# Kernel tuning notes

Hardware: AMD Instinct MI355X
Metric: run time of the kernel (lower is better)

The kernel has to match this reference:

```python
import jax, jax.numpy as jnp
import numpy as np

NUM_HEADS = 16
BN_EPS = 1e-3  # tf.layers.BatchNormalization default epsilon


def _z_norm(a, axis, scale):
    mu = jnp.mean(a, axis=axis, keepdims=True)
    sd = jnp.std(a, axis=axis, keepdims=True)
    return (a - mu) / (sd * scale + 1e-10)


def setup_inputs() -> dict:
    key = jax.random.key(0)
    ks = jax.random.split(key, 12)
    B, S, D = 4, 1024, 1024
    w = lambda k: jax.random.normal(k, (D, D), dtype=jnp.float32) * 0.02
    return {
        'q': jax.random.normal(ks[0], (B, S, D), dtype=jnp.float32),
        'k': jax.random.normal(ks[1], (B, S, D), dtype=jnp.float32),
        'v': jax.random.normal(ks[2], (B, S, D), dtype=jnp.float32),
        'mask': jax.random.randint(ks[3], (B, 1, S, S), 0, 2, dtype=jnp.int32),
        'is_training': 0,
        'q_gamma': jnp.ones((D,), jnp.float32),
        'q_beta': jnp.zeros((D,), jnp.float32),
        'q_mean': jax.random.normal(ks[4], (D,), dtype=jnp.float32) * 0.1,
        'q_var': jnp.ones((D,), jnp.float32),
        'Wq': w(ks[5]), 'bq': jnp.zeros((D,), jnp.float32),
        'Wqq': w(ks[6]), 'bqq': jnp.zeros((D,), jnp.float32),
        'Wo': w(ks[7]), 'bo': jnp.zeros((D,), jnp.float32),
    }


def reference(q, k, v, mask, is_training, q_gamma, q_beta, q_mean, q_var,
              Wq, bq, Wqq, bqq, Wo, bo):
    B, S, D = q.shape
    H = NUM_HEADS
    dh = D // H
    # BatchNorm (inference mode: call() passes no training flag -> moving stats)
    x = (q - q_mean) * jax.lax.rsqrt(q_var + BN_EPS) * q_gamma + q_beta
    # q = wqq(relu(wq(.)))  (k/v projections are dead: call() sets k = v = q)
    x = jax.nn.relu(x @ Wq + bq)
    x = x @ Wqq + bqq
    qh = x.reshape(B, S, H, dh).transpose(0, 2, 1, 3)  # [B,H,S,dh]
    logits = jnp.einsum('bhqd,bhkd->bhqk', qh, qh) / jnp.sqrt(jnp.float32(dh))
    logits = logits + mask.astype(logits.dtype) * -1e9
    attn = jax.nn.softmax(logits, axis=3)  # [B,H,S,S]
    last = jnp.mean(logits, axis=-1, keepdims=True)        # [B,H,S,1]
    last2 = jnp.mean(logits, axis=(2, 3), keepdims=True)   # [B,H,1,1]
    w_within = jax.nn.softmax(_z_norm(last, 2, 2), axis=2)   # softmax over queries
    w_betw = jax.nn.softmax(_z_norm(last2, 1, 2), axis=1)    # softmax over heads
    attn = attn * w_within * w_betw
    out = jnp.einsum('bhqk,bhkd->bhqd', attn, qh)           # v == qh
    out = out.transpose(0, 2, 1, 3).reshape(B, S, D)
    out = out @ Wo + bo
    return out, attn
```

## Files before the change

### kernel.cpp

```cpp
#include <hip/hip_runtime.h>
#include <math.h>


constexpr int Bz = 4, S = 1024, D = 1024, H = 16, DH = 64;
constexpr int N_ROWS = Bz * S;
#define BN_EPS 1e-3f
#define NEG_BIG -1e9f

typedef __attribute__((ext_vector_type(8))) short bf16x8;
typedef __attribute__((ext_vector_type(8))) unsigned short u16x8;
typedef __attribute__((ext_vector_type(4))) float f32x4;

__device__ inline unsigned short f2bf(float f) {
  union { float f; unsigned int u; } v; v.f = f;
  unsigned int u = v.u;
  return (unsigned short)((u + 0x7FFFu + ((u >> 16) & 1u)) >> 16);
}
__device__ inline float bf2f(unsigned short h) {
  union { unsigned int u; float f; } v; v.u = ((unsigned int)h) << 16;
  return v.f;
}
__device__ inline bf16x8 pack8(float4 a, float4 b) {
  bf16x8 v;
  v[0] = (short)f2bf(a.x); v[1] = (short)f2bf(a.y);
  v[2] = (short)f2bf(a.z); v[3] = (short)f2bf(a.w);
  v[4] = (short)f2bf(b.x); v[5] = (short)f2bf(b.y);
  v[6] = (short)f2bf(b.z); v[7] = (short)f2bf(b.w);
  return v;
}
__device__ inline float4 bnf(float4 f, float4 s, float4 sh) {
  return make_float4(fmaf(f.x, s.x, sh.x), fmaf(f.y, s.y, sh.y),
                     fmaf(f.z, s.z, sh.z), fmaf(f.w, s.w, sh.w));
}

__global__ __launch_bounds__(256)
void k_prep_all(const float* __restrict__ W0, const float* __restrict__ W1,
                const float* __restrict__ W2, unsigned short* __restrict__ T0,
                unsigned short* __restrict__ T1, unsigned short* __restrict__ T2,
                const float* __restrict__ gamma, const float* __restrict__ beta,
                const float* __restrict__ mean, const float* __restrict__ var,
                float* __restrict__ bnsc, float* __restrict__ bnsh,
                const int* __restrict__ mask, float* __restrict__ n_cnt2,
                float* __restrict__ cs) {
  __shared__ float Ls[64][65];
  const int bid = blockIdx.x, t = threadIdx.x;
  if (bid < 768) {
    const int z = bid >> 8, rem = bid & 255;
    const float* W = z == 0 ? W0 : (z == 1 ? W1 : W2);
    unsigned short* T = z == 0 ? T0 : (z == 1 ? T1 : T2);
    const int k0 = (rem & 15) * 64, n0 = (rem >> 4) * 64;
    {
      const int r = t >> 2, c0 = (t & 3) * 16;
#pragma unroll
      for (int i = 0; i < 4; ++i) {
        float4 f = *(const float4*)&W[(size_t)(k0 + r) * 1024 + n0 + c0 + 4 * i];
        Ls[r][c0 + 4 * i] = f.x; Ls[r][c0 + 4 * i + 1] = f.y;
        Ls[r][c0 + 4 * i + 2] = f.z; Ls[r][c0 + 4 * i + 3] = f.w;
      }
    }
    __syncthreads();
    {
      const int d = t >> 2, c = t & 3;
      u16x8 o0, o1;
#pragma unroll
      for (int i = 0; i < 8; ++i) {
        o0[i] = f2bf(Ls[c * 16 + i][d]);
        o1[i] = f2bf(Ls[c * 16 + 8 + i][d]);
      }
      unsigned short* dst = &T[(size_t)(n0 + d) * 1024 + k0 + c * 16];
      *(u16x8*)dst = o0;
      *(u16x8*)(dst + 8) = o1;
    }
  } else if (bid < 832) {
    const int id = bid - 768;
    const int row = id * 64 + (t >> 2);
    const int4* mp = (const int4*)&mask[(size_t)row * 1024 + (t & 3) * 256];
    int s = 0;
#pragma unroll 8
    for (int i = 0; i < 64; ++i) { int4 m = mp[i]; s += (m.x + m.y) + (m.z + m.w); }
    s += __shfl_xor(s, 1, 64);
    s += __shfl_xor(s, 2, 64);
    if ((t & 3) == 0) n_cnt2[row] = (float)s;
  } else if (bid < 836) {
    const int id = bid - 832;
    *(float4*)&cs[id * 1024 + t * 4] = make_float4(0.f, 0.f, 0.f, 0.f);
  } else {
    const int i = (bid - 836) * 256 + t;
    float sc = gamma[i] * rsqrtf(var[i] + BN_EPS);
    bnsc[i] = sc;
    bnsh[i] = beta[i] - mean[i] * sc;
  }
}

template<int AMODE, bool RELU, bool OUTBF, bool CSUM>
__global__ __launch_bounds__(256)
void k_gemm2n(const void* __restrict__ Asrc, const unsigned short* __restrict__ BT,
              const float* __restrict__ bias, void* __restrict__ C,
              const float* __restrict__ bnsc, const float* __restrict__ bnsh,
              float* __restrict__ cs) {
  __shared__ unsigned short As[128 * 64];
  __shared__ unsigned short Bs[64 * 64];
  const int t = threadIdx.x;
  const int w = t >> 6, l = t & 63, l15 = l & 15, l4 = l >> 4;
  const int m0 = blockIdx.x * 128, n0 = blockIdx.y * 64;
  const int wm = (w >> 1) * 64, wn = (w & 1) * 32;

  f32x4 acc[4][2];
#pragma unroll
  for (int i = 0; i < 4; ++i)
#pragma unroll
    for (int j = 0; j < 2; ++j) acc[i][j] = (f32x4){0.f, 0.f, 0.f, 0.f};

  for (int k0 = 0; k0 < 1024; k0 += 64) {
    __syncthreads();
#pragma unroll
    for (int i = 0; i < 4; ++i) {
      const int c = i * 256 + t, row = c >> 3, slot = c & 7;
      bf16x8 v;
      if (AMODE == 0) {
        v = *(const bf16x8*)&((const unsigned short*)Asrc)[(size_t)(m0 + row) * 1024 + k0 + slot * 8];
      } else {
        const float* ap = &((const float*)Asrc)[(size_t)(m0 + row) * 1024 + k0 + slot * 8];
        float4 f0 = *(const float4*)ap, f1 = *(const float4*)(ap + 4);
        float4 s0 = *(const float4*)&bnsc[k0 + slot * 8];
        float4 s1 = *(const float4*)&bnsc[k0 + slot * 8 + 4];
        float4 h0 = *(const float4*)&bnsh[k0 + slot * 8];
        float4 h1 = *(const float4*)&bnsh[k0 + slot * 8 + 4];
        v = pack8(bnf(f0, s0, h0), bnf(f1, s1, h1));
      }
      *(bf16x8*)((char*)As + row * 128 + ((slot * 16) ^ ((row & 7) << 4))) = v;
    }
#pragma unroll
    for (int i = 0; i < 2; ++i) {
      const int c = i * 256 + t, row = c >> 3, slot = c & 7;
      bf16x8 v = *(const bf16x8*)&BT[(size_t)(n0 + row) * 1024 + k0 + slot * 8];
      *(bf16x8*)((char*)Bs + row * 128 + ((slot * 16) ^ ((row & 7) << 4))) = v;
    }
    __syncthreads();
    bf16x8 af[4][2], bfr[2][2];
#pragma unroll
    for (int bm = 0; bm < 4; ++bm) {
      const int r = wm + bm * 16 + l15;
#pragma unroll
      for (int kk = 0; kk < 2; ++kk)
        af[bm][kk] = *(const bf16x8*)((const char*)As + r * 128 +
                                      ((kk * 64 + l4 * 16) ^ ((r & 7) << 4)));
    }
#pragma unroll
    for (int bn = 0; bn < 2; ++bn) {
      const int r = wn + bn * 16 + l15;
#pragma unroll
      for (int kk = 0; kk < 2; ++kk)
        bfr[bn][kk] = *(const bf16x8*)((const char*)Bs + r * 128 +
                                       ((kk * 64 + l4 * 16) ^ ((r & 7) << 4)));
    }
#pragma unroll
    for (int bm = 0; bm < 4; ++bm)
#pragma unroll
      for (int bn = 0; bn < 2; ++bn) {
        acc[bm][bn] = __builtin_amdgcn_mfma_f32_16x16x32_bf16(af[bm][0], bfr[bn][0], acc[bm][bn], 0, 0, 0);
        acc[bm][bn] = __builtin_amdgcn_mfma_f32_16x16x32_bf16(af[bm][1], bfr[bn][1], acc[bm][bn], 0, 0, 0);
      }
  }
  float bv[2];
#pragma unroll
  for (int bn = 0; bn < 2; ++bn) bv[bn] = bias[n0 + wn + bn * 16 + l15];
  float csum[2] = {0.f, 0.f};
#pragma unroll
  for (int bm = 0; bm < 4; ++bm)
#pragma unroll
    for (int bn = 0; bn < 2; ++bn)
#pragma unroll
      for (int r = 0; r < 4; ++r) {
        float v = acc[bm][bn][r] + bv[bn];
        if (RELU) v = fmaxf(v, 0.f);
        if (CSUM) csum[bn] += v;
        const size_t idx = (size_t)(m0 + wm + bm * 16 + l4 * 4 + r) * 1024 +
                           n0 + wn + bn * 16 + l15;
        if (OUTBF) ((unsigned short*)C)[idx] = f2bf(v);
        else ((float*)C)[idx] = v;
      }
  if (CSUM) {
#pragma unroll
    for (int bn = 0; bn < 2; ++bn) {
      float s = csum[bn];
      s += __shfl_xor(s, 16, 64);
      s += __shfl_xor(s, 32, 64);
      if (l4 == 0)
        atomicAdd(&cs[(m0 >> 10) * 1024 + n0 + wn + bn * 16 + l15], s);
    }
  }
}

__global__ __launch_bounds__(256)
void k_cvt(const unsigned short* __restrict__ xqb, unsigned short* __restrict__ qhT) {
  __shared__ unsigned short Ls[64][72];
  const int t = threadIdx.x;
  const int b = blockIdx.x >> 4;
  const int sb = (blockIdx.x & 15) * 64;
  const int h = blockIdx.y;
  {
    const int r = t >> 2, c0 = (t & 3) * 16;
    const unsigned short* src = &xqb[(size_t)(b * 1024 + sb + r) * 1024 + h * 64 + c0];
    u16x8 a = *(const u16x8*)src;
    u16x8 b8 = *(const u16x8*)(src + 8);
    *(u16x8*)&Ls[r][c0] = a;
    *(u16x8*)&Ls[r][c0 + 8] = b8;
  }
  __syncthreads();
  {
    const int d = t >> 2, c = t & 3;
    u16x8 o0, o1;
#pragma unroll
    for (int i = 0; i < 8; ++i) {
      o0[i] = Ls[c * 16 + i][d];
      o1[i] = Ls[c * 16 + 8 + i][d];
    }
    unsigned short* dst = &qhT[(size_t)((b * 16 + h) * 64 + d) * 1024 + sb + c * 16];
    *(u16x8*)dst = o0;
    *(u16x8*)(dst + 8) = o1;
  }
}

template<int PASS>
__global__ __launch_bounds__(256)
void k_attn6(const unsigned short* __restrict__ xqb, const int* __restrict__ mask,
             const unsigned short* __restrict__ qhT, const float* __restrict__ w_row,
             float* __restrict__ attn, unsigned short* __restrict__ pvb,
             float* __restrict__ denom) {
  __shared__ unsigned short Ks[2][128 * 64];
  __shared__ unsigned short Pst[PASS ? 4 * 16 * 64 : 8];

  const int t = threadIdx.x;
  const int w = t >> 6, l = t & 63;
  const int l15 = l & 15, l4 = l >> 4;
  const int q0 = blockIdx.x * 64;
  const int h = blockIdx.y, b = blockIdx.z;
  const int bh = b * 16 + h;

  bf16x8 qa0, qa1;
  {
    const unsigned short* qp =
        &xqb[(size_t)(b * 1024 + q0 + w * 16 + l15) * 1024 + h * 64 + l4 * 8];
    qa0 = *(const bf16x8*)qp;
    qa1 = *(const bf16x8*)(qp + 32);
  }

  float wsc[4];
  if (PASS == 1) {
#pragma unroll
    for (int r = 0; r < 4; ++r)
      wsc[r] = w_row[(size_t)bh * 1024 + q0 + w * 16 + l4 * 4 + r];
  }

  float dsum[4] = {0.f, 0.f, 0.f, 0.f};
  f32x4 vacc[4];
#pragma unroll
  for (int c = 0; c < 4; ++c) vacc[c] = (f32x4){0.f, 0.f, 0.f, 0.f};

  const int srow = t >> 3, sslot = t & 7;
  const int sswz = (sslot * 16) ^ ((srow & 7) << 4);
  const size_t sga = (size_t)(b * 1024 + srow) * 1024 + h * 64 + sslot * 8;

  bf16x8 s0, s1, s2, s3;
  s0 = *(const bf16x8*)&xqb[sga];
  s1 = *(const bf16x8*)&xqb[sga + 32 * 1024];
  s2 = *(const bf16x8*)&xqb[sga + 64 * 1024];
  s3 = *(const bf16x8*)&xqb[sga + 96 * 1024];
  *(bf16x8*)((char*)Ks[0] + srow * 128 + sswz) = s0;
  *(bf16x8*)((char*)Ks[0] + (srow + 32) * 128 + sswz) = s1;
  *(bf16x8*)((char*)Ks[0] + (srow + 64) * 128 + sswz) = s2;
  *(bf16x8*)((char*)Ks[0] + (srow + 96) * 128 + sswz) = s3;
  s0 = *(const bf16x8*)&xqb[sga + 128 * 1024];
  s1 = *(const bf16x8*)&xqb[sga + 160 * 1024];
  s2 = *(const bf16x8*)&xqb[sga + 192 * 1024];
  s3 = *(const bf16x8*)&xqb[sga + 224 * 1024];

  for (int ti = 0; ti < 8; ++ti) {
    __syncthreads();
    const int cur = ti & 1;
    if (ti < 7) {
      *(bf16x8*)((char*)Ks[cur ^ 1] + srow * 128 + sswz) = s0;
      *(bf16x8*)((char*)Ks[cur ^ 1] + (srow + 32) * 128 + sswz) = s1;
      *(bf16x8*)((char*)Ks[cur ^ 1] + (srow + 64) * 128 + sswz) = s2;
      *(bf16x8*)((char*)Ks[cur ^ 1] + (srow + 96) * 128 + sswz) = s3;
    }
    if (ti < 6) {
      const size_t base = sga + (size_t)(ti + 2) * 131072;
      s0 = *(const bf16x8*)&xqb[base];
      s1 = *(const bf16x8*)&xqb[base + 32 * 1024];
      s2 = *(const bf16x8*)&xqb[base + 64 * 1024];
      s3 = *(const bf16x8*)&xqb[base + 96 * 1024];
    }
    const int k0 = ti * 128;

#pragma unroll
    for (int half = 0; half < 2; ++half) {
      const int koff = k0 + half * 64;
      f32x4 lacc[4];
#pragma unroll
      for (int c = 0; c < 4; ++c) {
        const int r = half * 64 + c * 16 + l15;
        const char* kb = (const char*)Ks[cur] + r * 128;
        const int rsw = (r & 7) << 4;
        bf16x8 kb0 = *(const bf16x8*)(kb + ((l4 * 16) ^ rsw));
        bf16x8 kb1 = *(const bf16x8*)(kb + ((64 + l4 * 16) ^ rsw));
        f32x4 z = (f32x4){0.f, 0.f, 0.f, 0.f};
        z = __builtin_amdgcn_mfma_f32_16x16x32_bf16(qa0, kb0, z, 0, 0, 0);
        z = __builtin_amdgcn_mfma_f32_16x16x32_bf16(qa1, kb1, z, 0, 0, 0);
        lacc[c] = z;
      }

      int mrr[4][4];
#pragma unroll
      for (int c = 0; c < 4; ++c)
#pragma unroll
        for (int r = 0; r < 4; ++r)
          mrr[c][r] = mask[(size_t)(b * 1024 + q0 + w * 16 + l4 * 4 + r) * 1024 +
                           koff + c * 16 + l15];

#pragma unroll
      for (int c = 0; c < 4; ++c) {
#pragma unroll
        for (int r = 0; r < 4; ++r) {
          float p = __expf(fmaf((float)mrr[c][r], NEG_BIG, lacc[c][r] * 0.125f));
          if (PASS == 0) {
            dsum[r] += p;
          } else {
            attn[(size_t)(bh * 1024 + q0 + w * 16 + l4 * 4 + r) * 1024 +
                 koff + c * 16 + l15] = p * wsc[r];
            const int qq = l4 * 4 + r;
            *(unsigned short*)((char*)&Pst[w * 1024] + qq * 128 +
                               (((c * 16 + l15) * 2) ^ ((qq & 7) << 4))) = f2bf(p);
          }
        }
      }

      if (PASS == 1) {
#pragma unroll
        for (int kk = 0; kk < 2; ++kk) {
          const char* pb = (const char*)&Pst[w * 1024] + l15 * 128;
          bf16x8 pa = *(const bf16x8*)(pb + ((kk * 64 + l4 * 16) ^ ((l15 & 7) << 4)));
#pragma unroll
          for (int c = 0; c < 4; ++c) {
            bf16x8 vb = *(const bf16x8*)&qhT[(size_t)(bh * 64 + c * 16 + l15) * 1024 +
                                             koff + kk * 32 + l4 * 8];
            vacc[c] = __builtin_amdgcn_mfma_f32_16x16x32_bf16(pa, vb, vacc[c], 0, 0, 0);
          }
        }
      }
    }
  }

  if (PASS == 0) {
#pragma unroll
    for (int r = 0; r < 4; ++r) {
      float d2 = dsum[r];
#pragma unroll
      for (int m = 1; m < 16; m <<= 1) d2 += __shfl_xor(d2, m, 64);
      if (l15 == 0)
        denom[(size_t)bh * 1024 + q0 + w * 16 + l4 * 4 + r] = d2;
    }
  } else {
#pragma unroll
    for (int c = 0; c < 4; ++c)
#pragma unroll
      for (int r = 0; r < 4; ++r)
        pvb[(size_t)(b * 1024 + q0 + w * 16 + l4 * 4 + r) * 1024 +
            h * 64 + c * 16 + l15] = f2bf(vacc[c][r] * wsc[r]);
  }
}

__global__ __launch_bounds__(256)
void k_wwithin(const unsigned short* __restrict__ xqb, const float* __restrict__ cs,
               const float* __restrict__ n_cnt2, const float* __restrict__ denom,
               float* __restrict__ w_row) {
  __shared__ double buf[1024];
  __shared__ double red[256];
  __shared__ float csl[64];
  __shared__ double sh_mu, sh_sd, sh_zm, sh_es;
  const int bh = blockIdx.x, t = threadIdx.x;
  const int base = bh << 10;
  const int b = bh >> 4, h = bh & 15;
  const int nbase = b << 10;
  if (t < 64) csl[t] = cs[b * 1024 + h * 64 + t];
  __syncthreads();
  double part = 0;
  for (int j = 0; j < 4; ++j) {
    const int q2 = t + j * 256;
    const unsigned short* xr = &xqb[(size_t)(b * 1024 + q2) * 1024 + h * 64];
    float s = 0.f;
#pragma unroll
    for (int dd = 0; dd < 64; dd += 8) {
      u16x8 xv = *(const u16x8*)&xr[dd];
      s += bf2f(xv[0]) * csl[dd]     + bf2f(xv[1]) * csl[dd + 1] +
           bf2f(xv[2]) * csl[dd + 2] + bf2f(xv[3]) * csl[dd + 3] +
           bf2f(xv[4]) * csl[dd + 4] + bf2f(xv[5]) * csl[dd + 5] +
           bf2f(xv[6]) * csl[dd + 6] + bf2f(xv[7]) * csl[dd + 7];
    }
    double last = ((double)(s * 0.125f) - 1e9 * (double)n_cnt2[nbase + q2]) * (1.0 / 1024.0);
    buf[q2] = last; part += last;
  }
  red[t] = part; __syncthreads();
  for (int s2 = 128; s2 > 0; s2 >>= 1) { if (t < s2) red[t] += red[t + s2]; __syncthreads(); }
  if (t == 0) sh_mu = red[0] * (1.0 / 1024.0);
  __syncthreads();
  const double mu = sh_mu;
  part = 0;
  for (int q2 = t; q2 < 1024; q2 += 256) { double d = buf[q2] - mu; part += d * d; }
  red[t] = part; __syncthreads();
  for (int s2 = 128; s2 > 0; s2 >>= 1) { if (t < s2) red[t] += red[t + s2]; __syncthreads(); }
  if (t == 0) sh_sd = sqrt(red[0] * (1.0 / 1024.0));
  __syncthreads();
  const double dn = sh_sd * 2.0 + 1e-10;
  part = -1e300;
  for (int q2 = t; q2 < 1024; q2 += 256) {
    double z = (buf[q2] - mu) / dn;
    buf[q2] = z;
    part = fmax(part, z);
  }
  red[t] = part; __syncthreads();
  for (int s2 = 128; s2 > 0; s2 >>= 1) { if (t < s2) red[t] = fmax(red[t], red[t + s2]); __syncthreads(); }
  if (t == 0) sh_zm = red[0];
  __syncthreads();
  const double zm = sh_zm;
  part = 0;
  for (int q2 = t; q2 < 1024; q2 += 256) {
    double e = exp(buf[q2] - zm);
    buf[q2] = e; part += e;
  }
  red[t] = part; __syncthreads();
  for (int s2 = 128; s2 > 0; s2 >>= 1) { if (t < s2) red[t] += red[t + s2]; __syncthreads(); }
  if (t == 0) sh_es = red[0];
  __syncthreads();
  const double tot = sh_es;
  for (int q2 = t; q2 < 1024; q2 += 256) {
    w_row[base + q2] = (float)(buf[q2] / tot * 0.0625 / (double)denom[base + q2]);
  }
}

extern "C" void kernel_launch(void* const* d_in, const int* in_sizes, int n_in,
                              void* d_out, int out_size, void* d_ws, size_t ws_size,
                              hipStream_t stream) {
  const float* q      = (const float*)d_in[0];
  const int*   mask   = (const int*)d_in[3];
  const float* q_gamma = (const float*)d_in[5];
  const float* q_beta  = (const float*)d_in[6];
  const float* q_mean  = (const float*)d_in[7];
  const float* q_var   = (const float*)d_in[8];
  const float* Wq  = (const float*)d_in[9];
  const float* bq  = (const float*)d_in[10];
  const float* Wqq = (const float*)d_in[11];
  const float* bqq = (const float*)d_in[12];
  const float* Wo  = (const float*)d_in[13];
  const float* bo  = (const float*)d_in[14];

  float* out  = (float*)d_out;
  float* attn = (float*)d_out + (size_t)N_ROWS * D;
  unsigned short* xqb = (unsigned short*)d_out;

  char* ws = (char*)d_ws;
  unsigned short* x1b = (unsigned short*)(ws);
  unsigned short* qhT = (unsigned short*)(ws + (8u << 20));
  unsigned short* pvb = (unsigned short*)(ws + (16u << 20));
  unsigned short* WqT  = (unsigned short*)(ws + (32u << 20));
  unsigned short* WqqT = (unsigned short*)(ws + (34u << 20));
  unsigned short* WoT  = (unsigned short*)(ws + (36u << 20));
  float* cs     = (float*)(ws + (38u << 20));
  float* denom  = cs + 4096;
  float* w_row  = denom + 65536;
  float* n_cnt2 = w_row + 65536;
  float* bnsc   = n_cnt2 + 4096;
  float* bnsh   = bnsc + 1024;

  k_prep_all<<<840, 256, 0, stream>>>(Wq, Wqq, Wo, WqT, WqqT, WoT,
                                      q_gamma, q_beta, q_mean, q_var, bnsc, bnsh,
                                      mask, n_cnt2, cs);

  dim3 gg(32, 16);
  k_gemm2n<1, true, true, false><<<gg, 256, 0, stream>>>(q, WqT, bq, x1b, bnsc, bnsh, nullptr);
  k_gemm2n<0, false, true, true><<<gg, 256, 0, stream>>>(x1b, WqqT, bqq, xqb, nullptr, nullptr, cs);

  k_cvt<<<dim3(64, 16), 256, 0, stream>>>(xqb, qhT);

  dim3 ga(16, 16, 4);
  k_attn6<0><<<ga, 256, 0, stream>>>(xqb, mask, nullptr, nullptr, nullptr, nullptr, denom);
  k_wwithin<<<Bz * H, 256, 0, stream>>>(xqb, cs, n_cnt2, denom, w_row);
  k_attn6<1><<<ga, 256, 0, stream>>>(xqb, mask, qhT, w_row, attn, pvb, nullptr);

  k_gemm2n<0, false, false, false><<<gg, 256, 0, stream>>>(pvb, WoT, bo, out, nullptr, nullptr, nullptr);
}
```

Measured before the change: 248.4 us.

## Use direct global-to-LDS loads for GEMM and attention K tiles

```diff
diff --git a/kernel.cpp b/kernel.cpp
--- a/kernel.cpp
+++ b/kernel.cpp
@@ -31,6 +31,13 @@
 __device__ inline float4 bnf(float4 f, float4 s, float4 sh) {
   return make_float4(fmaf(f.x, s.x, sh.x), fmaf(f.y, s.y, sh.y),
                      fmaf(f.z, s.z, sh.z), fmaf(f.w, s.w, sh.w));
+}
+
+__device__ __forceinline__ void gl16(const void* g, void* l) {
+  __builtin_amdgcn_global_load_lds(
+      (const __attribute__((address_space(1))) unsigned int*)(unsigned long long)g,
+      (__attribute__((address_space(3))) unsigned int*)(unsigned int)(unsigned long long)l,
+      16, 0, 0);
 }
 
 __global__ __launch_bounds__(256)
@@ -116,9 +123,10 @@
 #pragma unroll
     for (int i = 0; i < 4; ++i) {
       const int c = i * 256 + t, row = c >> 3, slot = c & 7;
-      bf16x8 v;
       if (AMODE == 0) {
-        v = *(const bf16x8*)&((const unsigned short*)Asrc)[(size_t)(m0 + row) * 1024 + k0 + slot * 8];
+        const char* gs = (const char*)&((const unsigned short*)Asrc)[(size_t)(m0 + row) * 1024 + k0] +
+                         ((slot * 16) ^ ((row & 7) << 4));
+        gl16(gs, (char*)As + (i * 256 + w * 64) * 16);
       } else {
         const float* ap = &((const float*)Asrc)[(size_t)(m0 + row) * 1024 + k0 + slot * 8];
         float4 f0 = *(const float4*)ap, f1 = *(const float4*)(ap + 4);
@@ -126,15 +134,16 @@
         float4 s1 = *(const float4*)&bnsc[k0 + slot * 8 + 4];
         float4 h0 = *(const float4*)&bnsh[k0 + slot * 8];
         float4 h1 = *(const float4*)&bnsh[k0 + slot * 8 + 4];
-        v = pack8(bnf(f0, s0, h0), bnf(f1, s1, h1));
-      }
-      *(bf16x8*)((char*)As + row * 128 + ((slot * 16) ^ ((row & 7) << 4))) = v;
+        bf16x8 v = pack8(bnf(f0, s0, h0), bnf(f1, s1, h1));
+        *(bf16x8*)((char*)As + row * 128 + ((slot * 16) ^ ((row & 7) << 4))) = v;
+      }
     }
 #pragma unroll
     for (int i = 0; i < 2; ++i) {
       const int c = i * 256 + t, row = c >> 3, slot = c & 7;
-      bf16x8 v = *(const bf16x8*)&BT[(size_t)(n0 + row) * 1024 + k0 + slot * 8];
-      *(bf16x8*)((char*)Bs + row * 128 + ((slot * 16) ^ ((row & 7) << 4))) = v;
+      const char* gs = (const char*)&BT[(size_t)(n0 + row) * 1024 + k0] +
+                       ((slot * 16) ^ ((row & 7) << 4));
+      gl16(gs, (char*)Bs + (i * 256 + w * 64) * 16);
     }
     __syncthreads();
     bf16x8 af[4][2], bfr[2][2];
@@ -258,39 +267,25 @@
 #pragma unroll
   for (int c = 0; c < 4; ++c) vacc[c] = (f32x4){0.f, 0.f, 0.f, 0.f};
 
-  const int srow = t >> 3, sslot = t & 7;
-  const int sswz = (sslot * 16) ^ ((srow & 7) << 4);
-  const size_t sga = (size_t)(b * 1024 + srow) * 1024 + h * 64 + sslot * 8;
-
-  bf16x8 s0, s1, s2, s3;
-  s0 = *(const bf16x8*)&xqb[sga];
-  s1 = *(const bf16x8*)&xqb[sga + 32 * 1024];
-  s2 = *(const bf16x8*)&xqb[sga + 64 * 1024];
-  s3 = *(const bf16x8*)&xqb[sga + 96 * 1024];
-  *(bf16x8*)((char*)Ks[0] + srow * 128 + sswz) = s0;
-  *(bf16x8*)((char*)Ks[0] + (srow + 32) * 128 + sswz) = s1;
-  *(bf16x8*)((char*)Ks[0] + (srow + 64) * 128 + sswz) = s2;
-  *(bf16x8*)((char*)Ks[0] + (srow + 96) * 128 + sswz) = s3;
-  s0 = *(const bf16x8*)&xqb[sga + 128 * 1024];
-  s1 = *(const bf16x8*)&xqb[sga + 160 * 1024];
-  s2 = *(const bf16x8*)&xqb[sga + 192 * 1024];
-  s3 = *(const bf16x8*)&xqb[sga + 224 * 1024];
+#pragma unroll
+  for (int i = 0; i < 4; ++i) {
+    const int c = i * 256 + t, row = c >> 3, slot = c & 7;
+    const char* gs = (const char*)&xqb[(size_t)(b * 1024 + row) * 1024 + h * 64] +
+                     ((slot * 16) ^ ((row & 7) << 4));
+    gl16(gs, (char*)Ks[0] + (i * 256 + w * 64) * 16);
+  }
 
   for (int ti = 0; ti < 8; ++ti) {
     __syncthreads();
     const int cur = ti & 1;
     if (ti < 7) {
-      *(bf16x8*)((char*)Ks[cur ^ 1] + srow * 128 + sswz) = s0;
-      *(bf16x8*)((char*)Ks[cur ^ 1] + (srow + 32) * 128 + sswz) = s1;
-      *(bf16x8*)((char*)Ks[cur ^ 1] + (srow + 64) * 128 + sswz) = s2;
-      *(bf16x8*)((char*)Ks[cur ^ 1] + (srow + 96) * 128 + sswz) = s3;
-    }
-    if (ti < 6) {
-      const size_t base = sga + (size_t)(ti + 2) * 131072;
-      s0 = *(const bf16x8*)&xqb[base];
-      s1 = *(const bf16x8*)&xqb[base + 32 * 1024];
-      s2 = *(const bf16x8*)&xqb[base + 64 * 1024];
-      s3 = *(const bf16x8*)&xqb[base + 96 * 1024];
+#pragma unroll
+      for (int i = 0; i < 4; ++i) {
+        const int c = i * 256 + t, row = c >> 3, slot = c & 7;
+        const char* gs = (const char*)&xqb[(size_t)(b * 1024 + (ti + 1) * 128 + row) * 1024 + h * 64] +
+                         ((slot * 16) ^ ((row & 7) << 4));
+        gl16(gs, (char*)Ks[cur ^ 1] + (i * 256 + w * 64) * 16);
+      }
     }
     const int k0 = ti * 128;
 
```

Measured after the change: 246.4 us, median of 2. Within noise of the previous version (-0.8%).
